# Kernel tuning notes

Measured on AMD Instinct MI355X. Metric: run time of the kernel, lower is better.

Reference implementation:

```python
import jax, jax.numpy as jnp
import numpy as np

B, T, DIM = 2, 2048, 2048
H, DH = 16, 128
QC, KVC = 512, 512
DD = 64  # decoupled rope dim


def _rope_freqs(t, dd, theta=10000.0):
    inv = 1.0 / (theta ** (np.arange(0, dd, 2, dtype=np.float32) / dd))  # [dd/2]
    ang = np.arange(t, dtype=np.float32)[:, None] * inv[None, :]         # [T, dd/2]
    return jnp.asarray(np.stack([np.cos(ang), np.sin(ang)], axis=-1))    # [T, dd/2, 2]


def setup_inputs() -> dict:
    key = jax.random.key(0)
    ks = jax.random.split(key, 10)
    def w(k, i, o):
        return jax.random.normal(k, (i, o), jnp.float32) / np.sqrt(i)
    x = jax.random.normal(ks[0], (B, T, DIM), jnp.float32)
    freqs_cis = _rope_freqs(T, DD)
    neg = jnp.float32(-1e9)
    mask = jnp.where(jnp.tril(jnp.ones((T, T), bool)), 0.0, neg).astype(jnp.float32)
    return {
        "x": x, "freqs_cis": freqs_cis, "mask": mask,
        "W_dq": w(ks[1], DIM, QC), "W_uq": w(ks[2], QC, H * DH),
        "W_dkv": w(ks[3], DIM, KVC), "W_uk": w(ks[4], KVC, H * DH),
        "W_uv": w(ks[5], KVC, H * DH), "W_qr": w(ks[6], QC, H * DD),
        "W_kr": w(ks[7], DIM, DD), "W_o": w(ks[8], H * DH, DIM),
    }


def _apply_rope(t, freqs_cis):
    # t: [B, T, H, DD]; freqs_cis: [T, DD/2, 2]
    tp = t.reshape(*t.shape[:-1], -1, 2)               # [B,T,H,DD/2,2]
    cos = freqs_cis[None, :, None, :, 0]
    sin = freqs_cis[None, :, None, :, 1]
    x1, x2 = tp[..., 0], tp[..., 1]
    rot = jnp.stack([x1 * cos - x2 * sin, x1 * sin + x2 * cos], axis=-1)
    return rot.reshape(t.shape)


def reference(x, freqs_cis, mask, W_dq, W_uq, W_dkv, W_uk, W_uv, W_qr, W_kr, W_o):
    q_c = x @ W_dq                                     # [B,T,QC]
    kv_c = x @ W_dkv                                   # [B,T,KVC]
    q_rope = (q_c @ W_qr).reshape(B, T, H, DD)
    kv_rope = jnp.broadcast_to((x @ W_kr)[:, :, None, :], (B, T, H, DD))
    q_rope = _apply_rope(q_rope, freqs_cis)
    kv_rope = _apply_rope(kv_rope, freqs_cis)
    q = (q_c @ W_uq).reshape(B, T, H, DH)
    k = (kv_c @ W_uk).reshape(B, T, H, DH)
    v = (kv_c @ W_uv).reshape(B, T, H, DH)
    q = jnp.concatenate([q, q_rope], axis=-1)          # [B,T,H,DH+DD]
    k = jnp.concatenate([k, kv_rope], axis=-1)
    scale = 1.0 / np.sqrt(DH + DD)
    scores = jnp.einsum("bqhd,bkhd->bhqk", q, k) * scale + mask[None, None]
    attn = jax.nn.softmax(scores, axis=-1)
    out = jnp.einsum("bhqk,bkhd->bqhd", attn, v).reshape(B, T, H * DH)
    return out @ W_o
```

## Files before the change

kernel.cpp:

```cpp
#include <hip/hip_runtime.h>
#include <hip/hip_bf16.h>
#include <cstdint>
#include <cstddef>

typedef __bf16 bf16_t;
typedef __attribute__((ext_vector_type(8))) __bf16 bf16x8;
typedef __attribute__((ext_vector_type(4))) __bf16 bf16x4;
typedef __attribute__((ext_vector_type(4))) float f32x4;

#define B_ 2
#define T_ 2048
#define DIM_ 2048
#define H_ 16
#define DH_ 128
#define DD_ 64
#define DQK_ 192
#define QSTRIDE_ 3072
#define BT_ 4096
#define SCALE_ 0.07216878364870322f

__device__ __forceinline__ void gload16(const void* g, void* lds) {
  __builtin_amdgcn_global_load_lds(
      (const __attribute__((address_space(1))) unsigned int*)g,
      (__attribute__((address_space(3))) unsigned int*)lds, 16, 0, 0);
}

struct bf16_4 { bf16_t a, b, c, d; };
__global__ void cast_f32_bf16(const float* __restrict__ in, bf16_t* __restrict__ out, int n4) {
  int i = blockIdx.x * blockDim.x + threadIdx.x;
  if (i >= n4) return;
  float4 v = ((const float4*)in)[i];
  bf16_4 r{(bf16_t)v.x, (bf16_t)v.y, (bf16_t)v.z, (bf16_t)v.w};
  ((bf16_4*)out)[i] = r;
}

__global__ void transpose_all(const float* __restrict__ Wdq, const float* __restrict__ Wdkv,
                              const float* __restrict__ Wkr, const float* __restrict__ Wuq,
                              const float* __restrict__ Wqr, const float* __restrict__ Wuk,
                              const float* __restrict__ Wuv, const float* __restrict__ Wo,
                              bf16_t* __restrict__ Bt1, bf16_t* __restrict__ Bt2,
                              bf16_t* __restrict__ Bt3, bf16_t* __restrict__ Wo_t) {
  __shared__ float tile[32][33];
  int id = blockIdx.x;
  const float* W; bf16_t* Wt; int K, N, Np, kt;
  if (id < 1024)      { W = Wdq;  Wt = Bt1;                          K = 2048; N = 512;  Np = 512;  kt = 64; }
  else if (id < 2048) { W = Wdkv; Wt = Bt1 + (size_t)512 * 2048;  id -= 1024; K = 2048; N = 512;  Np = 512;  kt = 64; }
  else if (id < 2304) { W = Wkr;  Wt = Bt1 + (size_t)1024 * 2048; id -= 2048; K = 2048; N = 64;   Np = 128;  kt = 64; }
  else if (id < 3328) { W = Wuq;  Wt = Bt2;                       id -= 2304; K = 512;  N = 2048; Np = 2048; kt = 16; }
  else if (id < 3840) { W = Wqr;  Wt = Bt2 + (size_t)2048 * 512;  id -= 3328; K = 512;  N = 1024; Np = 1024; kt = 16; }
  else if (id < 4864) { W = Wuk;  Wt = Bt3;                       id -= 3840; K = 512;  N = 2048; Np = 2048; kt = 16; }
  else if (id < 5888) { W = Wuv;  Wt = Bt3 + (size_t)2048 * 512;  id -= 4864; K = 512;  N = 2048; Np = 2048; kt = 16; }
  else                { W = Wo;   Wt = Wo_t;                      id -= 5888; K = 2048; N = 2048; Np = 2048; kt = 64; }
  int k0 = (id % kt) * 32, n0 = (id / kt) * 32;
  int tx = threadIdx.x, ty = threadIdx.y;
#pragma unroll
  for (int i = 0; i < 4; ++i) {
    int k = k0 + ty + i * 8, n = n0 + tx;
    float v = (k < K && n < N) ? W[(size_t)k * N + n] : 0.f;
    tile[ty + i * 8][tx] = v;
  }
  __syncthreads();
#pragma unroll
  for (int i = 0; i < 4; ++i) {
    int n = n0 + ty + i * 8, k = k0 + tx;
    if (n < Np && k < K) Wt[(size_t)n * K + k] = (bf16_t)tile[tx][ty + i * 8];
  }
}

__global__ void transpose_v(const bf16_t* __restrict__ V, bf16_t* __restrict__ Vt) {
  __shared__ bf16_t tile[64 * 64];
  int id = blockIdx.x;
  int t0 = (id & 31) * 64;
  int d0 = ((id >> 5) & 1) * 64;
  int bh = id >> 6;
  int b = bh >> 4, h = bh & 15;
  int t = threadIdx.x;
#pragma unroll
  for (int it = 0; it < 2; ++it) {
    int idx = it * 256 + t;
    int tt = idx >> 3, c = idx & 7;
    bf16x8 v = *(const bf16x8*)&V[(size_t)(b * T_ + t0 + tt) * 2048 + h * 128 + d0 + c * 8];
    int sw = (tt ^ (tt >> 3)) & 7;
    *(bf16x8*)((char*)tile + tt * 128 + 16 * (c ^ sw)) = v;
  }
  __syncthreads();
#pragma unroll
  for (int it = 0; it < 2; ++it) {
    int idx = it * 256 + t;
    int dr = idx >> 3, c = idx & 7;
    bf16_t tmp[8];
#pragma unroll
    for (int u = 0; u < 8; ++u) {
      int sw = (u ^ c) & 7;
      tmp[u] = *(const bf16_t*)((const char*)tile + (8 * c + u) * 128 + ((2 * dr) ^ (16 * sw)));
    }
    *(bf16x8*)&Vt[((size_t)bh * 128 + d0 + dr) * T_ + t0 + c * 8] = *(bf16x8*)tmp;
  }
}

template <int MODE>
__global__ __launch_bounds__(256) void gemm_bt(const bf16_t* __restrict__ A,
                                               const bf16_t* __restrict__ Bt,
                                               void* __restrict__ C0v,
                                               void* __restrict__ C1v,
                                               void* __restrict__ C2v,
                                               const float* __restrict__ fr,
                                               int M, int N, int K, int ldc) {
  __shared__ bf16_t As[128 * 64];
  __shared__ bf16_t Bs[128 * 64];
  const int t = threadIdx.x;
  const int w = t >> 6, l = t & 63, l15 = l & 15, lhi = l >> 4;
  const int m0 = blockIdx.y * 128, n0 = blockIdx.x * 128;
  const int wr = (w >> 1) * 64, wc = (w & 1) * 64;

  f32x4 zero = {0.f, 0.f, 0.f, 0.f};
  f32x4 acc[4][4];
#pragma unroll
  for (int m = 0; m < 4; ++m)
#pragma unroll
    for (int n = 0; n < 4; ++n) acc[m][n] = zero;

  const int srow = t >> 3;
  const int scol = (((t & 7) ^ (srow & 7)) << 3);
  const int ldst = t * 8;

  for (int k0 = 0; k0 < K; k0 += 64) {
#pragma unroll
    for (int j = 0; j < 4; ++j) {
      gload16(A + (size_t)(m0 + srow + j * 32) * K + k0 + scol, &As[ldst + j * 2048]);
      gload16(Bt + (size_t)(n0 + srow + j * 32) * K + k0 + scol, &Bs[ldst + j * 2048]);
    }
    __syncthreads();
#pragma unroll
    for (int kk = 0; kk < 2; ++kk) {
      const int xs = ((((kk << 2) + lhi) ^ (l15 & 7)) << 3);
      bf16x8 af[4], bfr[4];
#pragma unroll
      for (int m = 0; m < 4; ++m)
        af[m] = *(const bf16x8*)&As[(wr + m * 16 + l15) * 64 + xs];
#pragma unroll
      for (int n = 0; n < 4; ++n)
        bfr[n] = *(const bf16x8*)&Bs[(wc + n * 16 + l15) * 64 + xs];
#pragma unroll
      for (int m = 0; m < 4; ++m)
#pragma unroll
        for (int n = 0; n < 4; ++n)
          acc[m][n] = __builtin_amdgcn_mfma_f32_16x16x32_bf16(af[m], bfr[n], acc[m][n], 0, 0, 0);
    }
    __syncthreads();
  }

#pragma unroll
  for (int m = 0; m < 4; ++m) {
#pragma unroll
    for (int n = 0; n < 4; ++n) {
#pragma unroll
      for (int r = 0; r < 4; ++r) {
        int row = m0 + wr + m * 16 + lhi * 4 + r;
        int col = n0 + wc + n * 16 + l15;
        float v = acc[m][n][r];
        if (MODE == 1) {
          ((float*)C0v)[(size_t)row * ldc + col] = v;
        } else if (MODE == 3) {
          if (col < 512) {
            ((bf16_t*)C0v)[(size_t)row * 512 + col] = (bf16_t)v;
          } else if (col < 1024) {
            ((bf16_t*)C1v)[(size_t)row * 512 + (col - 512)] = (bf16_t)v;
          } else if (col < 1088) {
            float other = __shfl_xor(v, 1, 64);
            int tt = row & (T_ - 1);
            int j = (col - 1024) >> 1;
            float2 cs = ((const float2*)fr)[tt * 32 + j];
            float o = (col & 1) ? (other * cs.y + v * cs.x) : (v * cs.x - other * cs.y);
            float o2 = __shfl_xor(o, 1, 64);
            if (!(col & 1)) {
              union { bf16_t h2[2]; unsigned u; } pk;
              pk.h2[0] = (bf16_t)o;
              pk.h2[1] = (bf16_t)o2;
              bf16_t* Kb = (bf16_t*)C2v;
#pragma unroll
              for (int hh = 0; hh < H_; ++hh)
                *(unsigned*)&Kb[(size_t)row * QSTRIDE_ + hh * DQK_ + 128 + (col - 1024)] = pk.u;
            }
          }
        } else if (MODE == 4) {
          if (col < 2048) {
            ((bf16_t*)C0v)[(size_t)row * QSTRIDE_ + (col >> 7) * DQK_ + (col & 127)] =
                (bf16_t)(v * SCALE_);
          } else {
            float other = __shfl_xor(v, 1, 64);
            int tt = row & (T_ - 1);
            int j = (col & 63) >> 1;
            float2 cs = ((const float2*)fr)[tt * 32 + j];
            float o = (col & 1) ? (other * cs.y + v * cs.x) : (v * cs.x - other * cs.y);
            int hh = (col - 2048) >> 6;
            ((bf16_t*)C0v)[(size_t)row * QSTRIDE_ + hh * DQK_ + 128 + (col & 63)] =
                (bf16_t)(o * SCALE_);
          }
        } else if (MODE == 5) {
          if (col < 2048) ((bf16_t*)C0v)[(size_t)row * QSTRIDE_ + (col >> 7) * DQK_ + (col & 127)] = (bf16_t)v;
          else            ((bf16_t*)C1v)[(size_t)row * 2048 + (col - 2048)] = (bf16_t)v;
        }
      }
    }
  }
}

#define KLDB 200
#define VLDB 72
#define PLDB 68

__global__ __launch_bounds__(256, 2) void flash_attn3(const bf16_t* __restrict__ Q,
                                                      const bf16_t* __restrict__ Kb,
                                                      const bf16_t* __restrict__ Vt,
                                                      bf16_t* __restrict__ Ob) {
  __shared__ bf16_t Ks[64 * KLDB];
  __shared__ bf16_t Vs[128 * VLDB];
  __shared__ bf16_t Ps[4][16 * PLDB];

  const int t = threadIdx.x, w = t >> 6, l = t & 63, l15 = l & 15, lhi = l >> 4;
  const int id = blockIdx.x;
  const int xcd = id & 7, sub = id >> 3;
  const int bh = xcd * 4 + (sub >> 4);
  const int qp = sub & 15;
  const int b = bh >> 4, h = bh & 15;
  const int qa = qp, qb = 31 - qp;

  int rK[6], cK[6];
#pragma unroll
  for (int i = 0; i < 6; ++i) { int idx = i * 256 + t; rK[i] = idx / 24; cK[i] = idx % 24; }
  const int rVt = t >> 3, cV = t & 7;
  const bf16_t* kbase = Kb + (size_t)b * T_ * QSTRIDE_ + h * DQK_;
  const bf16_t* vbase = Vt + (size_t)bh * DH_ * T_;

  bf16x8 kreg[6], vreg[4];
#define LOAD_TILE(K0)                                                                      \
  do {                                                                                     \
    _Pragma("unroll") for (int i = 0; i < 6; ++i)                                          \
        kreg[i] = *(const bf16x8*)(kbase + (size_t)((K0) + rK[i]) * QSTRIDE_ + cK[i] * 8); \
    _Pragma("unroll") for (int i = 0; i < 4; ++i)                                          \
        vreg[i] = *(const bf16x8*)(vbase + (size_t)(i * 32 + rVt) * T_ + (K0) + cV * 8);   \
  } while (0)
#define WRITE_TILE()                                                                       \
  do {                                                                                     \
    _Pragma("unroll") for (int i = 0; i < 6; ++i)                                          \
        *(bf16x8*)&Ks[rK[i] * KLDB + cK[i] * 8] = kreg[i];                                 \
    _Pragma("unroll") for (int i = 0; i < 4; ++i)                                          \
        *(bf16x8*)&Vs[(i * 32 + rVt) * VLDB + cV * 8] = vreg[i];                           \
  } while (0)

  f32x4 zero = {0.f, 0.f, 0.f, 0.f};

  LOAD_TILE(0);
  WRITE_TILE();
  __syncthreads();

  for (int pass = 0; pass < 2; ++pass) {
    const int qt = pass ? qb : qa;

    bf16x8 qf[6];
    {
      const bf16_t* qrow = Q + ((size_t)(b * T_ + qt * 64 + w * 16 + l15)) * QSTRIDE_ + h * DQK_;
#pragma unroll
      for (int kc = 0; kc < 6; ++kc) qf[kc] = *(const bf16x8*)(qrow + kc * 32 + lhi * 8);
    }

    float m_r[4], l_r[4];
    f32x4 accO[8];
#pragma unroll
    for (int r = 0; r < 4; ++r) { m_r[r] = -1e30f; l_r[r] = 0.f; }
#pragma unroll
    for (int n = 0; n < 8; ++n) accO[n] = zero;

    for (int kt = 0; kt <= qt; ++kt) {
      const bool last = (kt == qt);
      const bool haveNext = !(pass == 1 && last);
      if (haveNext) LOAD_TILE(last ? 0 : (kt + 1) * 64);

      f32x4 s[4];
#pragma unroll
      for (int n = 0; n < 4; ++n) s[n] = zero;
      __builtin_amdgcn_s_setprio(1);
#pragma unroll
      for (int kc = 0; kc < 6; ++kc) {
#pragma unroll
        for (int n = 0; n < 4; ++n) {
          bf16x8 kf = *(const bf16x8*)&Ks[(n * 16 + l15) * KLDB + kc * 32 + lhi * 8];
          s[n] = __builtin_amdgcn_mfma_f32_16x16x32_bf16(qf[kc], kf, s[n], 0, 0, 0);
        }
      }
      __builtin_amdgcn_s_setprio(0);

      if (last) {
#pragma unroll
        for (int n = 0; n < 4; ++n)
#pragma unroll
          for (int r = 0; r < 4; ++r) {
            int qq = w * 16 + lhi * 4 + r;
            int kk = n * 16 + l15;
            if (kk > qq) s[n][r] = -1e30f;
          }
      }
      float pmax[4];
#pragma unroll
      for (int r = 0; r < 4; ++r) {
        float v = fmaxf(fmaxf(s[0][r], s[1][r]), fmaxf(s[2][r], s[3][r]));
#pragma unroll
        for (int off = 1; off < 16; off <<= 1) v = fmaxf(v, __shfl_xor(v, off, 64));
        pmax[r] = v;
      }
      bool need = (pmax[0] > m_r[0] + 8.0f) || (pmax[1] > m_r[1] + 8.0f) ||
                  (pmax[2] > m_r[2] + 8.0f) || (pmax[3] > m_r[3] + 8.0f);
      if (__any(need ? 1 : 0)) {
        float corr[4];
#pragma unroll
        for (int r = 0; r < 4; ++r) {
          float mn = fmaxf(m_r[r], pmax[r]);
          corr[r] = __expf(m_r[r] - mn);
          m_r[r] = mn;
          l_r[r] *= corr[r];
        }
#pragma unroll
        for (int n = 0; n < 8; ++n)
#pragma unroll
          for (int r = 0; r < 4; ++r) accO[n][r] *= corr[r];
      }
#pragma unroll
      for (int n = 0; n < 4; ++n)
#pragma unroll
        for (int r = 0; r < 4; ++r) {
          float p = __expf(s[n][r] - m_r[r]);
          l_r[r] += p;
          Ps[w][(lhi * 4 + r) * PLDB + n * 16 + l15] = (bf16_t)p;
        }

      __builtin_amdgcn_s_setprio(1);
#pragma unroll
      for (int kc = 0; kc < 2; ++kc) {
        bf16x4 p0 = *(const bf16x4*)&Ps[w][l15 * PLDB + kc * 32 + lhi * 8];
        bf16x4 p1 = *(const bf16x4*)&Ps[w][l15 * PLDB + kc * 32 + lhi * 8 + 4];
        bf16x8 pf = __builtin_shufflevector(p0, p1, 0, 1, 2, 3, 4, 5, 6, 7);
#pragma unroll
        for (int n = 0; n < 8; ++n) {
          bf16x8 vf = *(const bf16x8*)&Vs[(n * 16 + l15) * VLDB + kc * 32 + lhi * 8];
          accO[n] = __builtin_amdgcn_mfma_f32_16x16x32_bf16(pf, vf, accO[n], 0, 0, 0);
        }
      }
      __builtin_amdgcn_s_setprio(0);

      __syncthreads();
      if (haveNext) WRITE_TILE();
      __syncthreads();
    }

    {
      float inv[4];
#pragma unroll
      for (int r = 0; r < 4; ++r) {
        float v = l_r[r];
#pragma unroll
        for (int off = 1; off < 16; off <<= 1) v += __shfl_xor(v, off, 64);
        inv[r] = 1.0f / v;
      }
#pragma unroll
      for (int n = 0; n < 8; ++n)
#pragma unroll
        for (int r = 0; r < 4; ++r) {
          size_t row = (size_t)(b * T_ + qt * 64 + w * 16 + lhi * 4 + r);
          Ob[row * (H_ * DH_) + h * DH_ + n * 16 + l15] = (bf16_t)(accO[n][r] * inv[r]);
        }
    }
  }
#undef LOAD_TILE
#undef WRITE_TILE
}

extern "C" void kernel_launch(void* const* d_in, const int* in_sizes, int n_in,
                              void* d_out, int out_size, void* d_ws, size_t ws_size,
                              hipStream_t stream) {
  (void)in_sizes; (void)n_in; (void)out_size; (void)ws_size;
  const float* x    = (const float*)d_in[0];
  const float* fr   = (const float*)d_in[1];
  const float* Wdq  = (const float*)d_in[3];
  const float* Wuq  = (const float*)d_in[4];
  const float* Wdkv = (const float*)d_in[5];
  const float* Wuk  = (const float*)d_in[6];
  const float* Wuv  = (const float*)d_in[7];
  const float* Wqr  = (const float*)d_in[8];
  const float* Wkr  = (const float*)d_in[9];
  const float* Wo   = (const float*)d_in[10];
  float* out = (float*)d_out;

  char* ws = (char*)d_ws;
  size_t off = 0;
  auto alloc = [&](size_t bytes) -> void* {
    void* p = ws + off;
    off += (bytes + 255) & ~(size_t)255;
    return p;
  };
  bf16_t* x_bf   = (bf16_t*)alloc((size_t)BT_ * DIM_ * 2);
  bf16_t* Bt1    = (bf16_t*)alloc((size_t)1152 * 2048 * 2);
  bf16_t* Bt2    = (bf16_t*)alloc((size_t)3072 * 512 * 2);
  bf16_t* Bt3    = (bf16_t*)alloc((size_t)4096 * 512 * 2);
  bf16_t* Wo_t   = (bf16_t*)alloc((size_t)2048 * 2048 * 2);
  bf16_t* q_c    = (bf16_t*)alloc((size_t)BT_ * 512 * 2);
  bf16_t* kv_c   = (bf16_t*)alloc((size_t)BT_ * 512 * 2);
  bf16_t* Qbuf   = (bf16_t*)alloc((size_t)BT_ * QSTRIDE_ * 2);
  bf16_t* Kbuf   = (bf16_t*)alloc((size_t)BT_ * QSTRIDE_ * 2);
  bf16_t* Vbuf   = (bf16_t*)alloc((size_t)BT_ * 2048 * 2);
  bf16_t* Vt_g   = (bf16_t*)alloc((size_t)BT_ * 2048 * 2);
  bf16_t* AObuf  = (bf16_t*)alloc((size_t)BT_ * 2048 * 2);

  cast_f32_bf16<<<(BT_ * DIM_ / 4 + 255) / 256, 256, 0, stream>>>(x, x_bf, BT_ * DIM_ / 4);
  transpose_all<<<9984, dim3(32, 8), 0, stream>>>(Wdq, Wdkv, Wkr, Wuq, Wqr, Wuk, Wuv, Wo,
                                                  Bt1, Bt2, Bt3, Wo_t);

  gemm_bt<3><<<dim3(9, 32),  256, 0, stream>>>(x_bf, Bt1, q_c, kv_c, Kbuf, fr, BT_, 1088, 2048, 0);
  gemm_bt<4><<<dim3(24, 32), 256, 0, stream>>>(q_c,  Bt2, Qbuf, nullptr, nullptr, fr, BT_, 3072, 512, 0);
  gemm_bt<5><<<dim3(32, 32), 256, 0, stream>>>(kv_c, Bt3, Kbuf, Vbuf, nullptr, nullptr, BT_, 4096, 512, 0);

  transpose_v<<<2048, 256, 0, stream>>>(Vbuf, Vt_g);

  flash_attn3<<<512, 256, 0, stream>>>(Qbuf, Kbuf, Vt_g, AObuf);

  gemm_bt<1><<<dim3(16, 32), 256, 0, stream>>>(AObuf, Wo_t, out, nullptr, nullptr, nullptr, BT_, 2048, 2048, 2048);
}
```

Measured before the change: 294.1 us.

## Use 128-row query tiles per block so each K/V tile feeds two query sub-tiles

The flash attention kernel now gives each block one 128-row query tile instead of two paired 64-row tiles processed in sequence. Each wave holds two 16-row query fragments and issues two MFMAs per K/V fragment read from shared memory, halving LDS traffic per unit of work. Work is balanced by a new block-index mapping that pairs tiles across a bh split and applies an XOR swizzle. In exchange, register pressure roughly doubles for accumulators and Q fragments, and the upper waves sit idle on the final diagonal tile.

```diff
diff --git a/kernel.cpp b/kernel.cpp
--- a/kernel.cpp
+++ b/kernel.cpp
@@ -210,21 +210,24 @@
 #define VLDB 72
 #define PLDB 68
 
-__global__ __launch_bounds__(256, 2) void flash_attn3(const bf16_t* __restrict__ Q,
+__global__ __launch_bounds__(256, 2) void flash_attn7(const bf16_t* __restrict__ Q,
                                                       const bf16_t* __restrict__ Kb,
                                                       const bf16_t* __restrict__ Vt,
                                                       bf16_t* __restrict__ Ob) {
   __shared__ bf16_t Ks[64 * KLDB];
   __shared__ bf16_t Vs[128 * VLDB];
-  __shared__ bf16_t Ps[4][16 * PLDB];
+  __shared__ bf16_t Ps[4][32 * PLDB];
 
   const int t = threadIdx.x, w = t >> 6, l = t & 63, l15 = l & 15, lhi = l >> 4;
   const int id = blockIdx.x;
-  const int xcd = id & 7, sub = id >> 3;
-  const int bh = xcd * 4 + (sub >> 4);
-  const int qp = sub & 15;
+  const int uu = id >> 1, pp = id & 1;
+  const int bh = (pp << 4) | (uu >> 4);
+  const int g = (uu & 15) ^ ((uu >> 7) ? 15 : 0);
+  const int qt = pp ? (15 - g) : g;
   const int b = bh >> 4, h = bh & 15;
-  const int qa = qp, qb = 31 - qp;
+  const int nkt = 2 * qt + 2;
+  const int myLast = 2 * qt + (w >= 2 ? 1 : 0);
+  const int qoff = (w >= 2) ? 64 : 0;
 
   int rK[6], cK[6];
 #pragma unroll
@@ -251,125 +254,153 @@
 
   f32x4 zero = {0.f, 0.f, 0.f, 0.f};
 
+  bf16x8 qf[2][6];
+#pragma unroll
+  for (int u = 0; u < 2; ++u) {
+    const bf16_t* qrow =
+        Q + ((size_t)(b * T_ + qt * 128 + w * 32 + u * 16 + l15)) * QSTRIDE_ + h * DQK_;
+#pragma unroll
+    for (int kc = 0; kc < 6; ++kc) qf[u][kc] = *(const bf16x8*)(qrow + kc * 32 + lhi * 8);
+  }
+
+  float m_r[2][4], l_r[2][4];
+  f32x4 accO[2][8];
+#pragma unroll
+  for (int u = 0; u < 2; ++u) {
+#pragma unroll
+    for (int r = 0; r < 4; ++r) { m_r[u][r] = -1e30f; l_r[u][r] = 0.f; }
+#pragma unroll
+    for (int n = 0; n < 8; ++n) accO[u][n] = zero;
+  }
+
   LOAD_TILE(0);
   WRITE_TILE();
   __syncthreads();
 
-  for (int pass = 0; pass < 2; ++pass) {
-    const int qt = pass ? qb : qa;
-
-    bf16x8 qf[6];
-    {
-      const bf16_t* qrow = Q + ((size_t)(b * T_ + qt * 64 + w * 16 + l15)) * QSTRIDE_ + h * DQK_;
-#pragma unroll
-      for (int kc = 0; kc < 6; ++kc) qf[kc] = *(const bf16x8*)(qrow + kc * 32 + lhi * 8);
-    }
-
-    float m_r[4], l_r[4];
-    f32x4 accO[8];
-#pragma unroll
-    for (int r = 0; r < 4; ++r) { m_r[r] = -1e30f; l_r[r] = 0.f; }
-#pragma unroll
-    for (int n = 0; n < 8; ++n) accO[n] = zero;
-
-    for (int kt = 0; kt <= qt; ++kt) {
-      const bool last = (kt == qt);
-      const bool haveNext = !(pass == 1 && last);
-      if (haveNext) LOAD_TILE(last ? 0 : (kt + 1) * 64);
-
-      f32x4 s[4];
-#pragma unroll
-      for (int n = 0; n < 4; ++n) s[n] = zero;
+  for (int kt = 0; kt < nkt; ++kt) {
+    const bool lastStep = (kt == nkt - 1);
+    if (!lastStep) LOAD_TILE((kt + 1) * 64);
+
+    if (kt <= myLast) {
+      const bool diag = (kt == myLast);
+
+      f32x4 s[2][4];
+#pragma unroll
+      for (int u = 0; u < 2; ++u)
+#pragma unroll
+        for (int n = 0; n < 4; ++n) s[u][n] = zero;
       __builtin_amdgcn_s_setprio(1);
 #pragma unroll
       for (int kc = 0; kc < 6; ++kc) {
 #pragma unroll
         for (int n = 0; n < 4; ++n) {
           bf16x8 kf = *(const bf16x8*)&Ks[(n * 16 + l15) * KLDB + kc * 32 + lhi * 8];
-          s[n] = __builtin_amdgcn_mfma_f32_16x16x32_bf16(qf[kc], kf, s[n], 0, 0, 0);
+          s[0][n] = __builtin_amdgcn_mfma_f32_16x16x32_bf16(qf[0][kc], kf, s[0][n], 0, 0, 0);
+          s[1][n] = __builtin_amdgcn_mfma_f32_16x16x32_bf16(qf[1][kc], kf, s[1][n], 0, 0, 0);
         }
       }
       __builtin_amdgcn_s_setprio(0);
 
-      if (last) {
+      if (diag) {
+#pragma unroll
+        for (int u = 0; u < 2; ++u)
+#pragma unroll
+          for (int n = 0; n < 4; ++n)
+#pragma unroll
+            for (int r = 0; r < 4; ++r) {
+              int qq = w * 32 + u * 16 + lhi * 4 + r - qoff;
+              int kk = n * 16 + l15;
+              if (kk > qq) s[u][n][r] = -1e30f;
+            }
+      }
+      float pmax[2][4];
+#pragma unroll
+      for (int u = 0; u < 2; ++u)
+#pragma unroll
+        for (int r = 0; r < 4; ++r) {
+          float v = fmaxf(fmaxf(s[u][0][r], s[u][1][r]), fmaxf(s[u][2][r], s[u][3][r]));
+#pragma unroll
+          for (int off = 1; off < 16; off <<= 1) v = fmaxf(v, __shfl_xor(v, off, 64));
+          pmax[u][r] = v;
+        }
+      bool need = false;
+#pragma unroll
+      for (int u = 0; u < 2; ++u)
+#pragma unroll
+        for (int r = 0; r < 4; ++r) need = need || (pmax[u][r] > m_r[u][r] + 8.0f);
+      if (__any(need ? 1 : 0)) {
+#pragma unroll
+        for (int u = 0; u < 2; ++u) {
+          float corr[4];
+#pragma unroll
+          for (int r = 0; r < 4; ++r) {
+            float mn = fmaxf(m_r[u][r], pmax[u][r]);
+            corr[r] = __expf(m_r[u][r] - mn);
+            m_r[u][r] = mn;
+            l_r[u][r] *= corr[r];
+          }
+#pragma unroll
+          for (int n = 0; n < 8; ++n)
+#pragma unroll
+            for (int r = 0; r < 4; ++r) accO[u][n][r] *= corr[r];
+        }
+      }
+#pragma unroll
+      for (int u = 0; u < 2; ++u)
 #pragma unroll
         for (int n = 0; n < 4; ++n)
 #pragma unroll
           for (int r = 0; r < 4; ++r) {
-            int qq = w * 16 + lhi * 4 + r;
-            int kk = n * 16 + l15;
-            if (kk > qq) s[n][r] = -1e30f;
+            float p = __expf(s[u][n][r] - m_r[u][r]);
+            l_r[u][r] += p;
+            Ps[w][(u * 16 + lhi * 4 + r) * PLDB + n * 16 + l15] = (bf16_t)p;
           }
-      }
-      float pmax[4];
-#pragma unroll
-      for (int r = 0; r < 4; ++r) {
-        float v = fmaxf(fmaxf(s[0][r], s[1][r]), fmaxf(s[2][r], s[3][r]));
-#pragma unroll
-        for (int off = 1; off < 16; off <<= 1) v = fmaxf(v, __shfl_xor(v, off, 64));
-        pmax[r] = v;
-      }
-      bool need = (pmax[0] > m_r[0] + 8.0f) || (pmax[1] > m_r[1] + 8.0f) ||
-                  (pmax[2] > m_r[2] + 8.0f) || (pmax[3] > m_r[3] + 8.0f);
-      if (__any(need ? 1 : 0)) {
-        float corr[4];
-#pragma unroll
-        for (int r = 0; r < 4; ++r) {
-          float mn = fmaxf(m_r[r], pmax[r]);
-          corr[r] = __expf(m_r[r] - mn);
-          m_r[r] = mn;
-          l_r[r] *= corr[r];
-        }
-#pragma unroll
-        for (int n = 0; n < 8; ++n)
-#pragma unroll
-          for (int r = 0; r < 4; ++r) accO[n][r] *= corr[r];
-      }
-#pragma unroll
-      for (int n = 0; n < 4; ++n)
-#pragma unroll
-        for (int r = 0; r < 4; ++r) {
-          float p = __expf(s[n][r] - m_r[r]);
-          l_r[r] += p;
-          Ps[w][(lhi * 4 + r) * PLDB + n * 16 + l15] = (bf16_t)p;
-        }
 
       __builtin_amdgcn_s_setprio(1);
 #pragma unroll
       for (int kc = 0; kc < 2; ++kc) {
-        bf16x4 p0 = *(const bf16x4*)&Ps[w][l15 * PLDB + kc * 32 + lhi * 8];
-        bf16x4 p1 = *(const bf16x4*)&Ps[w][l15 * PLDB + kc * 32 + lhi * 8 + 4];
-        bf16x8 pf = __builtin_shufflevector(p0, p1, 0, 1, 2, 3, 4, 5, 6, 7);
+        bf16x8 pf[2];
+#pragma unroll
+        for (int u = 0; u < 2; ++u) {
+          const bf16_t* pb = &Ps[w][(u * 16 + l15) * PLDB + kc * 32 + lhi * 8];
+          bf16x4 p0 = *(const bf16x4*)pb;
+          bf16x4 p1 = *(const bf16x4*)(pb + 4);
+          pf[u] = __builtin_shufflevector(p0, p1, 0, 1, 2, 3, 4, 5, 6, 7);
+        }
 #pragma unroll
         for (int n = 0; n < 8; ++n) {
           bf16x8 vf = *(const bf16x8*)&Vs[(n * 16 + l15) * VLDB + kc * 32 + lhi * 8];
-          accO[n] = __builtin_amdgcn_mfma_f32_16x16x32_bf16(pf, vf, accO[n], 0, 0, 0);
+          accO[0][n] = __builtin_amdgcn_mfma_f32_16x16x32_bf16(pf[0], vf, accO[0][n], 0, 0, 0);
+          accO[1][n] = __builtin_amdgcn_mfma_f32_16x16x32_bf16(pf[1], vf, accO[1][n], 0, 0, 0);
         }
       }
       __builtin_amdgcn_s_setprio(0);
-
+    }
+
+    __syncthreads();
+    if (!lastStep) {
+      WRITE_TILE();
       __syncthreads();
-      if (haveNext) WRITE_TILE();
-      __syncthreads();
-    }
-
-    {
-      float inv[4];
+    }
+  }
+
+#pragma unroll
+  for (int u = 0; u < 2; ++u) {
+    float inv[4];
+#pragma unroll
+    for (int r = 0; r < 4; ++r) {
+      float v = l_r[u][r];
+#pragma unroll
+      for (int off = 1; off < 16; off <<= 1) v += __shfl_xor(v, off, 64);
+      inv[r] = 1.0f / v;
+    }
+#pragma unroll
+    for (int n = 0; n < 8; ++n)
 #pragma unroll
       for (int r = 0; r < 4; ++r) {
-        float v = l_r[r];
-#pragma unroll
-        for (int off = 1; off < 16; off <<= 1) v += __shfl_xor(v, off, 64);
-        inv[r] = 1.0f / v;
-      }
-#pragma unroll
-      for (int n = 0; n < 8; ++n)
-#pragma unroll
-        for (int r = 0; r < 4; ++r) {
-          size_t row = (size_t)(b * T_ + qt * 64 + w * 16 + lhi * 4 + r);
-          Ob[row * (H_ * DH_) + h * DH_ + n * 16 + l15] = (bf16_t)(accO[n][r] * inv[r]);
-        }
-    }
+        size_t row = (size_t)(b * T_ + qt * 128 + w * 32 + u * 16 + lhi * 4 + r);
+        Ob[row * (H_ * DH_) + h * DH_ + n * 16 + l15] = (bf16_t)(accO[u][n][r] * inv[r]);
+      }
   }
 #undef LOAD_TILE
 #undef WRITE_TILE
@@ -421,7 +452,7 @@
 
   transpose_v<<<2048, 256, 0, stream>>>(Vbuf, Vt_g);
 
-  flash_attn3<<<512, 256, 0, stream>>>(Qbuf, Kbuf, Vt_g, AObuf);
+  flash_attn7<<<512, 256, 0, stream>>>(Qbuf, Kbuf, Vt_g, AObuf);
 
   gemm_bt<1><<<dim3(16, 32), 256, 0, stream>>>(AObuf, Wo_t, out, nullptr, nullptr, nullptr, BT_, 2048, 2048, 2048);
 }
```

After: 325.4 us. 1.11x slower.
